# Performance work log

Measured on AMD Instinct MI355X. Metric: run time of the kernel, lower is better.

The kernel has to match this reference:

```python
import jax, jax.numpy as jnp
import numpy as np

FIELD_NUM = 24

def _pair_indices(f):
    ii, jj = np.triu_indices(f, k=1)
    return jnp.asarray(ii), jnp.asarray(jj)

def setup_inputs() -> dict:
    key = jax.random.key(0)
    k1, k2 = jax.random.split(key)
    B, F, D = 16384, FIELD_NUM, 64
    P = F * (F - 1) // 2  # 276
    x = jax.random.normal(k1, (B, F, D), dtype=jnp.float32)
    W = jax.random.normal(k2, (P, D, D), dtype=jnp.float32) * 0.05
    return {"x": x, "W": W}

def reference(x, W):
    # x: (B, F, D) field embeddings; W: (P, D, D) per-pair bilinear matrices
    idx_i, idx_j = _pair_indices(FIELD_NUM)
    xi = x[:, idx_i, :]  # (B, P, D)
    xj = x[:, idx_j, :]  # (B, P, D)
    # sum_{p,d,e} xi[b,p,d] * W[p,d,e] * xj[b,p,e]
    logit = jnp.einsum('bpd,pde,bpe->b', xi, W, xj)
    return logit[:, None]  # (B, 1), matching tf output shape
```

## Files before the change

### kernel.cpp

```cpp
#include <hip/hip_runtime.h>
#include <stdint.h>

#define B_TOT 16384
#define F_NUM 24
#define D_DIM 64
#define P_NUM 276
#define BT    32
#define ROWP  1544
#define NTH   512

typedef float f32x16 __attribute__((ext_vector_type(16)));
typedef short bf16x8 __attribute__((ext_vector_type(8)));

__device__ inline unsigned short f2bf(float f) {
    unsigned u = __float_as_uint(f);
    u += 0x7fffu + ((u >> 16) & 1u);
    return (unsigned short)(u >> 16);
}
__device__ inline float bf2f(unsigned short h) {
    return __uint_as_float(((unsigned)h) << 16);
}

struct WTab { int ent[8][36]; };
constexpr WTab build_tab() {
    WTab t{};
    const int fl[8][6] = {
        {0,12,-1,-1,-1,-1},
        {1,11,-1,-1,-1,-1},
        {2,10,-1,-1,-1,-1},
        {3, 9,-1,-1,-1,-1},
        {4, 8,-1,-1,-1,-1},
        {5, 7,-1,-1,-1,-1},
        {6,14,17,20,22,-1},
        {13,15,16,18,19,21}};
    for (int w = 0; w < 8; ++w) {
        int c = 0;
        for (int k = 0; k < 6; ++k) {
            int f = fl[w][k];
            if (f < 0) break;
            int base = 23 * f - f * (f - 1) / 2;
            for (int j = f + 1; j < 24; ++j)
                t.ent[w][c++] = (base + j - f - 1) | (j << 9) | (f << 14);
        }
        int last = t.ent[w][c - 1];
        while (c < 36) t.ent[w][c++] = last;
    }
    return t;
}
__device__ __constant__ WTab gtab = build_tab();

__global__ __launch_bounds__(256) void wprep(const float* __restrict__ W,
                                             unsigned short* __restrict__ afrag) {
    __shared__ __align__(16) unsigned short wlds[64 * 72];
    int p = blockIdx.x, t = threadIdx.x;
    const float4* src = (const float4*)(W + (size_t)p * 4096);
    #pragma unroll
    for (int c = 0; c < 4; ++c) {
        int i = t + c * 256;
        float4 v = src[i];
        int d = i >> 4;
        int e = (i & 15) * 4;
        ushort4 h; h.x=f2bf(v.x); h.y=f2bf(v.y); h.z=f2bf(v.z); h.w=f2bf(v.w);
        *(ushort4*)(&wlds[d * 72 + e]) = h;
    }
    __syncthreads();
    unsigned short* dst = afrag + (size_t)p * 4096;
    #pragma unroll
    for (int c = 0; c < 2; ++c) {
        int sl = t + c * 256;
        int u = sl >> 6, lane = sl & 63;
        int m = u & 1, ks = u >> 1;
        int d = m * 32 + (lane & 31);
        int e = ks * 16 + (lane >> 5) * 8;
        bf16x8 v = *(const bf16x8*)(&wlds[d * 72 + e]);
        *(bf16x8*)(dst + (size_t)sl * 8) = v;
    }
}

__global__ __launch_bounds__(NTH, 2) void fmfm_main(const float* __restrict__ x,
                                                    const unsigned short* __restrict__ afrag,
                                                    float* __restrict__ out) {
    __shared__ __align__(16) unsigned short xs[BT * ROWP];
    __shared__ float t_red[BT];
    int tid = threadIdx.x;
    int btile = blockIdx.x;

    const float4* xg = (const float4*)(x + (size_t)btile * BT * (F_NUM * D_DIM));
    #pragma unroll
    for (int c = 0; c < (BT * 384) / NTH; ++c) {
        int it = tid + c * NTH;
        int row = it / 384;
        int c4  = it % 384;
        float4 v = xg[it];
        ushort4 h; h.x=f2bf(v.x); h.y=f2bf(v.y); h.z=f2bf(v.z); h.w=f2bf(v.w);
        *(ushort4*)(&xs[row * ROWP + c4 * 4]) = h;
    }
    if (tid < BT) t_red[tid] = 0.0f;
    __syncthreads();

    int lane = tid & 63;
    int wv   = __builtin_amdgcn_readfirstlane(tid >> 6);
    int bcol = lane & 31;
    int q    = lane >> 5;
    int q8   = q * 8, q4 = q * 4;
    const unsigned short* xrow = xs + bcol * ROWP;
    int cnt = (wv < 6) ? 34 : 36;

    f32x16 acc0, acc1;
    #pragma unroll
    for (int i = 0; i < 16; ++i) { acc0[i] = 0.0f; acc1[i] = 0.0f; }
    float tacc = 0.0f;

    const bf16x8* afr = (const bf16x8*)afrag;

    auto epilogue = [&](int f) {
        int eb = f * 64 + q4;
        #pragma unroll
        for (int g = 0; g < 4; ++g) {
            ushort4 x0 = *(const ushort4*)(xrow + eb + 8 * g);
            ushort4 x1 = *(const ushort4*)(xrow + eb + 32 + 8 * g);
            tacc += acc0[4*g+0]*bf2f(x0.x) + acc0[4*g+1]*bf2f(x0.y)
                  + acc0[4*g+2]*bf2f(x0.z) + acc0[4*g+3]*bf2f(x0.w);
            tacc += acc1[4*g+0]*bf2f(x1.x) + acc1[4*g+1]*bf2f(x1.y)
                  + acc1[4*g+2]*bf2f(x1.z) + acc1[4*g+3]*bf2f(x1.w);
        }
        #pragma unroll
        for (int i = 0; i < 16; ++i) { acc0[i] = 0.0f; acc1[i] = 0.0f; }
    };

    auto step = [&](int s, bf16x8* buf) {
        int e = gtab.ent[wv][s];
        int j = (e >> 9) & 31;
        int f = e >> 14;
        const unsigned short* xb = xrow + j * 64 + q8;
        bf16x8 b0 = *(const bf16x8*)(xb);
        bf16x8 b1 = *(const bf16x8*)(xb + 16);
        bf16x8 b2 = *(const bf16x8*)(xb + 32);
        bf16x8 b3 = *(const bf16x8*)(xb + 48);
        acc0 = __builtin_amdgcn_mfma_f32_32x32x16_bf16(buf[0], b0, acc0, 0, 0, 0);
        acc1 = __builtin_amdgcn_mfma_f32_32x32x16_bf16(buf[1], b0, acc1, 0, 0, 0);
        acc0 = __builtin_amdgcn_mfma_f32_32x32x16_bf16(buf[2], b1, acc0, 0, 0, 0);
        acc1 = __builtin_amdgcn_mfma_f32_32x32x16_bf16(buf[3], b1, acc1, 0, 0, 0);
        acc0 = __builtin_amdgcn_mfma_f32_32x32x16_bf16(buf[4], b2, acc0, 0, 0, 0);
        acc1 = __builtin_amdgcn_mfma_f32_32x32x16_bf16(buf[5], b2, acc1, 0, 0, 0);
        acc0 = __builtin_amdgcn_mfma_f32_32x32x16_bf16(buf[6], b3, acc0, 0, 0, 0);
        acc1 = __builtin_amdgcn_mfma_f32_32x32x16_bf16(buf[7], b3, acc1, 0, 0, 0);
        int sp = (s + 2 < cnt) ? s + 2 : cnt - 1;
        int pp = gtab.ent[wv][sp] & 511;
        const bf16x8* ap = afr + (size_t)pp * 512 + lane;
        #pragma unroll
        for (int u = 0; u < 8; ++u) buf[u] = ap[u * 64];
        if (j == 23) epilogue(f);
    };

    bf16x8 bufA[8], bufB[8];
    {
        int p0 = gtab.ent[wv][0] & 511;
        const bf16x8* ap = afr + (size_t)p0 * 512 + lane;
        #pragma unroll
        for (int u = 0; u < 8; ++u) bufA[u] = ap[u * 64];
        int p1 = gtab.ent[wv][1] & 511;
        ap = afr + (size_t)p1 * 512 + lane;
        #pragma unroll
        for (int u = 0; u < 8; ++u) bufB[u] = ap[u * 64];
    }

    for (int s = 0; s < cnt; s += 2) {
        step(s,     bufA);
        step(s + 1, bufB);
    }

    atomicAdd(&t_red[bcol], tacc);
    __syncthreads();
    if (tid < BT) out[(size_t)btile * BT + tid] = t_red[tid];
}

extern "C" void kernel_launch(void* const* d_in, const int* in_sizes, int n_in,
                              void* d_out, int out_size, void* d_ws, size_t ws_size,
                              hipStream_t stream) {
    const float* x = (const float*)d_in[0];
    const float* W = (const float*)d_in[1];
    float* out = (float*)d_out;
    unsigned short* afrag = (unsigned short*)d_ws;
    wprep<<<P_NUM, 256, 0, stream>>>(W, afrag);
    fmfm_main<<<B_TOT / BT, NTH, 0, stream>>>(x, afrag, out);
}
```

Before: 192.0 us.

## Double batch tile and split the e-dimension so each W fragment serves two batch groups

Raises the batch tile from 32 to 64 rows and processes the inner e-dimension in two halves of 32. Only the current half of x is staged in LDS as bf16, which keeps the larger tile within shared memory. The W fragment layout is reordered by k-slice so each wave loads half a W tile per pair per phase and reuses it across two 32-row batch groups, halving W fragment traffic per batch. The epilogue now reads fp32 x straight from global memory instead of LDS. In exchange the grid shrinks to 256 blocks, which may lower occupancy, and each block adds an extra staging phase with its own barriers.

```diff
diff --git a/kernel.cpp b/kernel.cpp
--- a/kernel.cpp
+++ b/kernel.cpp
@@ -5,9 +5,9 @@
 #define F_NUM 24
 #define D_DIM 64
 #define P_NUM 276
-#define BT    32
-#define ROWP  1544
+#define BT    64
 #define NTH   512
+#define ROWS  770
 
 typedef float f32x16 __attribute__((ext_vector_type(16)));
 typedef short bf16x8 __attribute__((ext_vector_type(8)));
@@ -16,9 +16,6 @@
     unsigned u = __float_as_uint(f);
     u += 0x7fffu + ((u >> 16) & 1u);
     return (unsigned short)(u >> 16);
-}
-__device__ inline float bf2f(unsigned short h) {
-    return __uint_as_float(((unsigned)h) << 16);
 }
 
 struct WTab { int ent[8][36]; };
@@ -64,113 +61,131 @@
         *(ushort4*)(&wlds[d * 72 + e]) = h;
     }
     __syncthreads();
-    unsigned short* dst = afrag + (size_t)p * 4096;
     #pragma unroll
     for (int c = 0; c < 2; ++c) {
         int sl = t + c * 256;
         int u = sl >> 6, lane = sl & 63;
-        int m = u & 1, ks = u >> 1;
+        int ks = u >> 1, m = u & 1;
         int d = m * 32 + (lane & 31);
         int e = ks * 16 + (lane >> 5) * 8;
         bf16x8 v = *(const bf16x8*)(&wlds[d * 72 + e]);
-        *(bf16x8*)(dst + (size_t)sl * 8) = v;
+        size_t dst = ((size_t)((ks * P_NUM + p) * 2 + m) * 64 + lane) * 8;
+        *(bf16x8*)(afrag + dst) = v;
     }
 }
 
 __global__ __launch_bounds__(NTH, 2) void fmfm_main(const float* __restrict__ x,
                                                     const unsigned short* __restrict__ afrag,
                                                     float* __restrict__ out) {
-    __shared__ __align__(16) unsigned short xs[BT * ROWP];
+    __shared__ __align__(16) unsigned short xs[BT * ROWS];
     __shared__ float t_red[BT];
-    int tid = threadIdx.x;
-    int btile = blockIdx.x;
-
-    const float4* xg = (const float4*)(x + (size_t)btile * BT * (F_NUM * D_DIM));
+    const int tid = threadIdx.x;
+    const int btile = blockIdx.x;
+    const int lane = tid & 63;
+    const int wv = __builtin_amdgcn_readfirstlane(tid >> 6);
+    const int bcol = lane & 31;
+    const int q = lane >> 5;
+
+    if (tid < BT) t_red[tid] = 0.0f;
+
+    const int cnt = (wv < 6) ? 34 : 36;
+    const bf16x8* afr = (const bf16x8*)afrag;
+
+    float tacc0 = 0.0f, tacc1 = 0.0f;
+    f32x16 acc00, acc01, acc10, acc11;
     #pragma unroll
-    for (int c = 0; c < (BT * 384) / NTH; ++c) {
-        int it = tid + c * NTH;
-        int row = it / 384;
-        int c4  = it % 384;
-        float4 v = xg[it];
-        ushort4 h; h.x=f2bf(v.x); h.y=f2bf(v.y); h.z=f2bf(v.z); h.w=f2bf(v.w);
-        *(ushort4*)(&xs[row * ROWP + c4 * 4]) = h;
-    }
-    if (tid < BT) t_red[tid] = 0.0f;
-    __syncthreads();
-
-    int lane = tid & 63;
-    int wv   = __builtin_amdgcn_readfirstlane(tid >> 6);
-    int bcol = lane & 31;
-    int q    = lane >> 5;
-    int q8   = q * 8, q4 = q * 4;
-    const unsigned short* xrow = xs + bcol * ROWP;
-    int cnt = (wv < 6) ? 34 : 36;
-
-    f32x16 acc0, acc1;
-    #pragma unroll
-    for (int i = 0; i < 16; ++i) { acc0[i] = 0.0f; acc1[i] = 0.0f; }
-    float tacc = 0.0f;
-
-    const bf16x8* afr = (const bf16x8*)afrag;
-
-    auto epilogue = [&](int f) {
-        int eb = f * 64 + q4;
-        #pragma unroll
-        for (int g = 0; g < 4; ++g) {
-            ushort4 x0 = *(const ushort4*)(xrow + eb + 8 * g);
-            ushort4 x1 = *(const ushort4*)(xrow + eb + 32 + 8 * g);
-            tacc += acc0[4*g+0]*bf2f(x0.x) + acc0[4*g+1]*bf2f(x0.y)
-                  + acc0[4*g+2]*bf2f(x0.z) + acc0[4*g+3]*bf2f(x0.w);
-            tacc += acc1[4*g+0]*bf2f(x1.x) + acc1[4*g+1]*bf2f(x1.y)
-                  + acc1[4*g+2]*bf2f(x1.z) + acc1[4*g+3]*bf2f(x1.w);
-        }
-        #pragma unroll
-        for (int i = 0; i < 16; ++i) { acc0[i] = 0.0f; acc1[i] = 0.0f; }
-    };
-
-    auto step = [&](int s, bf16x8* buf) {
-        int e = gtab.ent[wv][s];
-        int j = (e >> 9) & 31;
-        int f = e >> 14;
-        const unsigned short* xb = xrow + j * 64 + q8;
-        bf16x8 b0 = *(const bf16x8*)(xb);
-        bf16x8 b1 = *(const bf16x8*)(xb + 16);
-        bf16x8 b2 = *(const bf16x8*)(xb + 32);
-        bf16x8 b3 = *(const bf16x8*)(xb + 48);
-        acc0 = __builtin_amdgcn_mfma_f32_32x32x16_bf16(buf[0], b0, acc0, 0, 0, 0);
-        acc1 = __builtin_amdgcn_mfma_f32_32x32x16_bf16(buf[1], b0, acc1, 0, 0, 0);
-        acc0 = __builtin_amdgcn_mfma_f32_32x32x16_bf16(buf[2], b1, acc0, 0, 0, 0);
-        acc1 = __builtin_amdgcn_mfma_f32_32x32x16_bf16(buf[3], b1, acc1, 0, 0, 0);
-        acc0 = __builtin_amdgcn_mfma_f32_32x32x16_bf16(buf[4], b2, acc0, 0, 0, 0);
-        acc1 = __builtin_amdgcn_mfma_f32_32x32x16_bf16(buf[5], b2, acc1, 0, 0, 0);
-        acc0 = __builtin_amdgcn_mfma_f32_32x32x16_bf16(buf[6], b3, acc0, 0, 0, 0);
-        acc1 = __builtin_amdgcn_mfma_f32_32x32x16_bf16(buf[7], b3, acc1, 0, 0, 0);
-        int sp = (s + 2 < cnt) ? s + 2 : cnt - 1;
-        int pp = gtab.ent[wv][sp] & 511;
-        const bf16x8* ap = afr + (size_t)pp * 512 + lane;
-        #pragma unroll
-        for (int u = 0; u < 8; ++u) buf[u] = ap[u * 64];
-        if (j == 23) epilogue(f);
-    };
-
-    bf16x8 bufA[8], bufB[8];
-    {
-        int p0 = gtab.ent[wv][0] & 511;
-        const bf16x8* ap = afr + (size_t)p0 * 512 + lane;
-        #pragma unroll
-        for (int u = 0; u < 8; ++u) bufA[u] = ap[u * 64];
-        int p1 = gtab.ent[wv][1] & 511;
-        ap = afr + (size_t)p1 * 512 + lane;
-        #pragma unroll
-        for (int u = 0; u < 8; ++u) bufB[u] = ap[u * 64];
-    }
-
-    for (int s = 0; s < cnt; s += 2) {
-        step(s,     bufA);
-        step(s + 1, bufB);
-    }
-
-    atomicAdd(&t_red[bcol], tacc);
+    for (int i = 0; i < 16; ++i) { acc00[i]=0.f; acc01[i]=0.f; acc10[i]=0.f; acc11[i]=0.f; }
+
+    const float* xg  = x + (size_t)btile * BT * 1536;
+    const float* xe0 = xg + (size_t)bcol * 1536 + 4 * q;
+    const float* xe1 = xe0 + (size_t)32 * 1536;
+    const unsigned short* xr0 = xs + bcol * ROWS;
+    const unsigned short* xr1 = xs + (bcol + 32) * ROWS;
+
+    for (int h = 0; h < 2; ++h) {
+        __syncthreads();
+        for (int k = 0; k < 24; ++k) {
+            int g = tid + k * NTH;
+            int row = g / 192;
+            int r = g - row * 192;
+            int f = r >> 3, i = r & 7;
+            float4 v = *(const float4*)(xg + (size_t)row * 1536 + f * 64 + h * 32 + i * 4);
+            ushort4 hh; hh.x=f2bf(v.x); hh.y=f2bf(v.y); hh.z=f2bf(v.z); hh.w=f2bf(v.w);
+            *(ushort4*)(&xs[row * ROWS + f * 32 + i * 4]) = hh;
+        }
+        __syncthreads();
+
+        const int ks0 = 2 * h;
+
+        auto epi = [&](int f) {
+            const float* e0 = xe0 + f * 64;
+            const float* e1 = xe1 + f * 64;
+            #pragma unroll
+            for (int g = 0; g < 4; ++g) {
+                float4 v = *(const float4*)(e0 + 8 * g);
+                tacc0 += acc00[4*g+0]*v.x + acc00[4*g+1]*v.y + acc00[4*g+2]*v.z + acc00[4*g+3]*v.w;
+                v = *(const float4*)(e0 + 32 + 8 * g);
+                tacc0 += acc01[4*g+0]*v.x + acc01[4*g+1]*v.y + acc01[4*g+2]*v.z + acc01[4*g+3]*v.w;
+                v = *(const float4*)(e1 + 8 * g);
+                tacc1 += acc10[4*g+0]*v.x + acc10[4*g+1]*v.y + acc10[4*g+2]*v.z + acc10[4*g+3]*v.w;
+                v = *(const float4*)(e1 + 32 + 8 * g);
+                tacc1 += acc11[4*g+0]*v.x + acc11[4*g+1]*v.y + acc11[4*g+2]*v.z + acc11[4*g+3]*v.w;
+            }
+            #pragma unroll
+            for (int i = 0; i < 16; ++i) { acc00[i]=0.f; acc01[i]=0.f; acc10[i]=0.f; acc11[i]=0.f; }
+        };
+
+        auto step = [&](int s, bf16x8* buf) {
+            int e = gtab.ent[wv][s];
+            int j = (e >> 9) & 31;
+            int f = e >> 14;
+            const unsigned short* a0 = xr0 + j * 32 + q * 8;
+            const unsigned short* a1 = xr1 + j * 32 + q * 8;
+            bf16x8 b00 = *(const bf16x8*)(a0);
+            bf16x8 b01 = *(const bf16x8*)(a0 + 16);
+            bf16x8 b10 = *(const bf16x8*)(a1);
+            bf16x8 b11 = *(const bf16x8*)(a1 + 16);
+            acc00 = __builtin_amdgcn_mfma_f32_32x32x16_bf16(buf[0], b00, acc00, 0, 0, 0);
+            acc01 = __builtin_amdgcn_mfma_f32_32x32x16_bf16(buf[1], b00, acc01, 0, 0, 0);
+            acc10 = __builtin_amdgcn_mfma_f32_32x32x16_bf16(buf[0], b10, acc10, 0, 0, 0);
+            acc11 = __builtin_amdgcn_mfma_f32_32x32x16_bf16(buf[1], b10, acc11, 0, 0, 0);
+            acc00 = __builtin_amdgcn_mfma_f32_32x32x16_bf16(buf[2], b01, acc00, 0, 0, 0);
+            acc01 = __builtin_amdgcn_mfma_f32_32x32x16_bf16(buf[3], b01, acc01, 0, 0, 0);
+            acc10 = __builtin_amdgcn_mfma_f32_32x32x16_bf16(buf[2], b11, acc10, 0, 0, 0);
+            acc11 = __builtin_amdgcn_mfma_f32_32x32x16_bf16(buf[3], b11, acc11, 0, 0, 0);
+            int sp = (s + 2 < cnt) ? s + 2 : cnt - 1;
+            int pp = gtab.ent[wv][sp] & 511;
+            #pragma unroll
+            for (int u = 0; u < 4; ++u) {
+                int ksl = u >> 1, m = u & 1;
+                buf[u] = afr[(size_t)(((ks0 + ksl) * P_NUM + pp) * 2 + m) * 64 + lane];
+            }
+            if (j == 23) epi(f);
+        };
+
+        bf16x8 bufA[4], bufB[4];
+        {
+            int p0 = gtab.ent[wv][0] & 511;
+            #pragma unroll
+            for (int u = 0; u < 4; ++u) {
+                int ksl = u >> 1, m = u & 1;
+                bufA[u] = afr[(size_t)(((ks0 + ksl) * P_NUM + p0) * 2 + m) * 64 + lane];
+            }
+            int p1 = gtab.ent[wv][1] & 511;
+            #pragma unroll
+            for (int u = 0; u < 4; ++u) {
+                int ksl = u >> 1, m = u & 1;
+                bufB[u] = afr[(size_t)(((ks0 + ksl) * P_NUM + p1) * 2 + m) * 64 + lane];
+            }
+        }
+        for (int s = 0; s < cnt; s += 2) {
+            step(s,     bufA);
+            step(s + 1, bufB);
+        }
+    }
+
+    atomicAdd(&t_red[bcol],      tacc0);
+    atomicAdd(&t_red[bcol + 32], tacc1);
     __syncthreads();
     if (tid < BT) out[(size_t)btile * BT + tid] = t_red[tid];
 }
```

Result: slower. 227.5 us (+18.4%).
